# Kernel tuning notes

Hardware: AMD Instinct MI355X
Metric: run time of the kernel (lower is better)

The kernel has to match this reference:

```python
import jax, jax.numpy as jnp
import numpy as np

B, T, I, H, L, O = 256, 512, 5, 100, 5, 3
BN_EPS = 1e-5


def _lstm_layer(xs, W_ih, W_hh, bias):
    """xs: [B,T,in] -> hidden seq [B,T,H]. PyTorch gate order i,f,g,o."""
    Bv = xs.shape[0]
    Hd = W_hh.shape[1]
    h0 = jnp.zeros((Bv, Hd), xs.dtype)
    c0 = jnp.zeros((Bv, Hd), xs.dtype)

    def step(carry, x_t):
        h, c = carry
        gates = x_t @ W_ih.T + h @ W_hh.T + bias  # [B,4H]
        i, f, g, o = jnp.split(gates, 4, axis=-1)
        i = jax.nn.sigmoid(i)
        f = jax.nn.sigmoid(f)
        g = jnp.tanh(g)
        o = jax.nn.sigmoid(o)
        c = f * c + i * g
        h = o * jnp.tanh(c)
        return (h, c), h

    _, hs = jax.lax.scan(step, (h0, c0), xs.transpose(1, 0, 2))  # hs: [T,B,H]
    return hs.transpose(1, 0, 2)


def setup_inputs() -> dict:
    key = jax.random.key(0)
    ks = jax.random.split(key, 12)
    s = 0.1  # weight scale to keep gates in a reasonable range
    return {
        "x": jax.random.normal(ks[0], (B, T, I), jnp.float32),
        "W_ih0": jax.random.normal(ks[1], (4 * H, I), jnp.float32) * s,
        "W_hh0": jax.random.normal(ks[2], (4 * H, H), jnp.float32) * s,
        "b0": jax.random.normal(ks[3], (4 * H,), jnp.float32) * s,
        "W_ih": jax.random.normal(ks[4], (L - 1, 4 * H, H), jnp.float32) * s,
        "W_hh": jax.random.normal(ks[5], (L - 1, 4 * H, H), jnp.float32) * s,
        "b": jax.random.normal(ks[6], (L - 1, 4 * H), jnp.float32) * s,
        "gamma": jnp.ones((H,), jnp.float32),
        "beta": jnp.zeros((H,), jnp.float32),
        "run_mean": jnp.zeros((H,), jnp.float32),
        "run_var": jnp.ones((H,), jnp.float32),
        "W1": jax.random.normal(ks[7], (H, H), jnp.float32) * s,
        "b1": jnp.zeros((H,), jnp.float32),
        "W2": jax.random.normal(ks[8], (H, H), jnp.float32) * s,
        "b2": jnp.zeros((H,), jnp.float32),
        "W3": jax.random.normal(ks[9], (O, H), jnp.float32) * s,
        "b3": jnp.zeros((O,), jnp.float32),
    }


def reference(x, W_ih0, W_hh0, b0, W_ih, W_hh, b,
              gamma, beta, run_mean, run_var,
              W1, b1, W2, b2, W3, b3):
    # 5-layer stacked LSTM (batch_first)
    h = _lstm_layer(x, W_ih0, W_hh0, b0)
    for l in range(L - 1):
        h = _lstm_layer(h, W_ih[l], W_hh[l], b[l])
    # dropout (eval mode -> identity), take last timestep
    last = h[:, -1, :]  # [B,H]
    # BatchNorm1d, eval mode (running statistics)
    xn = (last - run_mean) * jax.lax.rsqrt(run_var + BN_EPS) * gamma + beta
    # 3-layer MLP head with ReLU
    y = jax.nn.relu(xn @ W1.T + b1)
    y = jax.nn.relu(y @ W2.T + b2)
    return y @ W3.T + b3  # [B,O]
```

## Files before the change

### kernel.cpp

```cpp
#include <hip/hip_runtime.h>

#define NT 1024
#define TSEQ 512

typedef float float2v __attribute__((ext_vector_type(2)));

__device__ __forceinline__ float sigmoid_(float x) { return 1.0f / (1.0f + __expf(-x)); }
__device__ __forceinline__ float tanh_(float x) { return 1.0f - 2.0f / (1.0f + __expf(2.0f * x)); }

extern "C" __global__ void prep_weights(const float* __restrict__ Wih0,
                                        const float* __restrict__ Whh0,
                                        const float* __restrict__ WihL,
                                        const float* __restrict__ WhhL,
                                        float4* __restrict__ wbuf) {
    int gid = blockIdx.x * 256 + threadIdx.x;
    if (gid >= 102400) return;
    int tid = gid & 1023;
    int lgq = gid >> 10;
    int gq = lgq % 20;
    int l = lgq / 20;
    int g = gq / 5, q = gq % 5;
    float tmp[4] = {0.f, 0.f, 0.f, 0.f};
    if (tid < 1000) {
        int f = tid / 100, rg = tid % 100;
        int row = g * 100 + rg;
        int k0 = 20 * f + 4 * q;
        for (int c = 0; c < 4; ++c) {
            int k = k0 + c;
            float w = 0.f;
            if (l == 0) {
                if (k < 5) w = Wih0[row * 5 + k];
                else if (k < 105) w = Whh0[row * 100 + (k - 5)];
            } else {
                if (k < 100) w = WihL[(l - 1) * 40000 + row * 100 + k];
                else w = WhhL[(l - 1) * 40000 + row * 100 + (k - 100)];
            }
            tmp[c] = w;
        }
    }
    wbuf[gid] = make_float4(tmp[0], tmp[1], tmp[2], tmp[3]);
}

template <int IN, bool FIRST, bool STORE>
__device__ void run_layer(const float4* __restrict__ wl, const float* __restrict__ bL,
                          const float* __restrict__ xsrc, float* __restrict__ hdst,
                          int b, int tid, int f, int rg, bool real,
                          float* xh, float4* part4) {
    float2v w[40];
#pragma unroll
    for (int g = 0; g < 4; ++g) {
#pragma unroll
        for (int q = 0; q < 5; ++q) {
            float4 t = wl[(g * 5 + q) * 1024 + tid];
            w[g * 10 + 2 * q]     = (float2v){t.x, t.y};
            w[g * 10 + 2 * q + 1] = (float2v){t.z, t.w};
        }
    }
    float bi = 0.f, bf = 0.f, bg = 0.f, bo = 0.f;
    if (tid < 100) {
        bi = bL[tid]; bf = bL[100 + tid]; bg = bL[200 + tid]; bo = bL[300 + tid];
    }

    if (tid < 256) xh[tid] = 0.f;
    __syncthreads();
    if (FIRST) {
        if (tid < 5) xh[tid] = xsrc[b * TSEQ * 5 + tid];
    } else {
        if (tid < 25) ((float4*)xh)[tid] = ((const float4*)xsrc)[b * TSEQ * 25 + tid];
    }
    __syncthreads();

    const float4* xv4 = (const float4*)xh + f * 5;
    float c = 0.f, hprev = 0.f;

    for (int t = 0; t < TSEQ; ++t) {
        if (STORE) {
            if (tid < 100 && t > 0) hdst[(b * TSEQ + (t - 1)) * 100 + tid] = hprev;
        }
        int tn = (t + 1 < TSEQ) ? (t + 1) : (TSEQ - 1);
        float pfs = 0.f;
        float4 pf4 = {0.f, 0.f, 0.f, 0.f};
        if (FIRST) {
            if (tid >= 128 && tid < 133) pfs = xsrc[(b * TSEQ + tn) * 5 + (tid - 128)];
        } else {
            if (tid >= 128 && tid < 153) pf4 = ((const float4*)xsrc)[(b * TSEQ + tn) * 25 + (tid - 128)];
        }

        float2v a0 = {0.f, 0.f}, a1 = {0.f, 0.f}, a2 = {0.f, 0.f}, a3 = {0.f, 0.f};
#pragma unroll
        for (int q = 0; q < 5; ++q) {
            float4 xq = xv4[q];
            float2v xlo = (float2v){xq.x, xq.y};
            float2v xhi = (float2v){xq.z, xq.w};
            a0 = __builtin_elementwise_fma(w[2 * q],      xlo, a0);
            a0 = __builtin_elementwise_fma(w[2 * q + 1],  xhi, a0);
            a1 = __builtin_elementwise_fma(w[10 + 2 * q],     xlo, a1);
            a1 = __builtin_elementwise_fma(w[10 + 2 * q + 1], xhi, a1);
            a2 = __builtin_elementwise_fma(w[20 + 2 * q],     xlo, a2);
            a2 = __builtin_elementwise_fma(w[20 + 2 * q + 1], xhi, a2);
            a3 = __builtin_elementwise_fma(w[30 + 2 * q],     xlo, a3);
            a3 = __builtin_elementwise_fma(w[30 + 2 * q + 1], xhi, a3);
        }
        if (real) {
            part4[f * 100 + rg] = make_float4(a0.x + a0.y, a1.x + a1.y,
                                              a2.x + a2.y, a3.x + a3.y);
        }
        __syncthreads();

        if (tid < 100) {
            float4 s = part4[tid];
#pragma unroll
            for (int ff = 1; ff < 10; ++ff) {
                float4 tt = part4[ff * 100 + tid];
                s.x += tt.x; s.y += tt.y; s.z += tt.z; s.w += tt.w;
            }
            float gi = sigmoid_(s.x + bi);
            float gf = sigmoid_(s.y + bf);
            float gg = tanh_(s.z + bg);
            float go = sigmoid_(s.w + bo);
            c = gf * c + gi * gg;
            float hv = go * tanh_(c);
            xh[IN + tid] = hv;
            hprev = hv;
        }
        if (FIRST) {
            if (tid >= 128 && tid < 133) xh[tid - 128] = pfs;
        } else {
            if (tid >= 128 && tid < 153) ((float4*)xh)[tid - 128] = pf4;
        }
        __syncthreads();
    }
    if (STORE) {
        if (tid < 100) hdst[(b * TSEQ + TSEQ - 1) * 100 + tid] = hprev;
    }
}

extern "C" __global__ void __launch_bounds__(NT, 4)
gesture_lstm_kernel(const float* __restrict__ x,
                    const float4* __restrict__ wbuf,
                    const float* __restrict__ b0, const float* __restrict__ bLv,
                    const float* __restrict__ gamma, const float* __restrict__ beta,
                    const float* __restrict__ rmean, const float* __restrict__ rvar,
                    const float* __restrict__ W1, const float* __restrict__ b1,
                    const float* __restrict__ W2, const float* __restrict__ b2,
                    const float* __restrict__ W3, const float* __restrict__ b3,
                    float* __restrict__ out, float* __restrict__ hseq) {
    __shared__ __align__(16) float xh[256];
    __shared__ __align__(16) float4 part4[1000];
    __shared__ __align__(16) float hw[10000];

    int tid = threadIdx.x;
    int b = blockIdx.x;
    int f = tid / 100;
    int rg = tid % 100;
    bool real = tid < 1000;

    run_layer<5,   true,  true >(wbuf + 0 * 20480, b0,         x,    hseq, b, tid, f, rg, real, xh, part4);
    run_layer<100, false, true >(wbuf + 1 * 20480, bLv + 0,    hseq, hseq, b, tid, f, rg, real, xh, part4);
    run_layer<100, false, true >(wbuf + 2 * 20480, bLv + 400,  hseq, hseq, b, tid, f, rg, real, xh, part4);
    run_layer<100, false, true >(wbuf + 3 * 20480, bLv + 800,  hseq, hseq, b, tid, f, rg, real, xh, part4);
    run_layer<100, false, false>(wbuf + 4 * 20480, bLv + 1200, hseq, hseq, b, tid, f, rg, real, xh, part4);

    float* fcbuf = (float*)part4;
    if (tid < 100) {
        float hv = xh[100 + tid];
        xh[tid] = (hv - rmean[tid]) * rsqrtf(rvar[tid] + 1e-5f) * gamma[tid] + beta[tid];
    }
    __syncthreads();

    for (int i = tid; i < 2500; i += NT) ((float4*)hw)[i] = ((const float4*)W1)[i];
    __syncthreads();
    if (tid < 100) {
        float acc = b1[tid];
#pragma unroll
        for (int k = 0; k < 100; ++k) acc = fmaf(hw[tid * 100 + k], xh[k], acc);
        fcbuf[tid] = fmaxf(acc, 0.0f);
    }
    __syncthreads();

    for (int i = tid; i < 2500; i += NT) ((float4*)hw)[i] = ((const float4*)W2)[i];
    __syncthreads();
    if (tid < 100) {
        float acc = b2[tid];
#pragma unroll
        for (int k = 0; k < 100; ++k) acc = fmaf(hw[tid * 100 + k], fcbuf[k], acc);
        fcbuf[400 + tid] = fmaxf(acc, 0.0f);
    }
    __syncthreads();

    if (tid < 3) {
        float acc = b3[tid];
#pragma unroll
        for (int k = 0; k < 100; ++k) acc = fmaf(W3[tid * 100 + k], fcbuf[400 + k], acc);
        out[b * 3 + tid] = acc;
    }
}

extern "C" void kernel_launch(void* const* d_in, const int* in_sizes, int n_in,
                              void* d_out, int out_size, void* d_ws, size_t ws_size,
                              hipStream_t stream) {
    const float* x     = (const float*)d_in[0];
    const float* Wih0  = (const float*)d_in[1];
    const float* Whh0  = (const float*)d_in[2];
    const float* b0    = (const float*)d_in[3];
    const float* WihL  = (const float*)d_in[4];
    const float* WhhL  = (const float*)d_in[5];
    const float* bLv   = (const float*)d_in[6];
    const float* gamma = (const float*)d_in[7];
    const float* beta  = (const float*)d_in[8];
    const float* rmean = (const float*)d_in[9];
    const float* rvar  = (const float*)d_in[10];
    const float* W1    = (const float*)d_in[11];
    const float* b1    = (const float*)d_in[12];
    const float* W2    = (const float*)d_in[13];
    const float* b2    = (const float*)d_in[14];
    const float* W3    = (const float*)d_in[15];
    const float* b3    = (const float*)d_in[16];

    float4* wbuf = (float4*)d_ws;
    float* hseq  = (float*)((char*)d_ws + 102400 * 16);

    prep_weights<<<dim3(400), dim3(256), 0, stream>>>(Wih0, Whh0, WihL, WhhL, wbuf);
    gesture_lstm_kernel<<<dim3(256), dim3(NT), 0, stream>>>(
        x, wbuf, b0, bLv, gamma, beta, rmean, rvar, W1, b1, W2, b2, W3, b3,
        (float*)d_out, hseq);
}
```

Baseline: 2.433 ms.

## Halve LSTM workgroup to 512 threads with 40-wide K slices

Reworks the per-sample LSTM workgroup from 1024 to 512 threads. Each thread now holds 80 float2 weight registers covering a 40-wide K slice, so the cross-slice reduction sums 5 partials instead of 10. The input-projection slices read x_t directly from global memory into registers, prefetched one step ahead, instead of staging it through shared memory. A lighter custom barrier replaces __syncthreads, and hidden-state stores are issued per step by the owner threads. The aim is to cut reduction and barrier cost per timestep, at the price of heavier register pressure (launch bounds lowered to 2) and more serial FMA work per thread.

```diff
diff --git a/kernel.cpp b/kernel.cpp
--- a/kernel.cpp
+++ b/kernel.cpp
@@ -1,12 +1,18 @@
 #include <hip/hip_runtime.h>
 
-#define NT 1024
+#define NT 512
 #define TSEQ 512
 
 typedef float float2v __attribute__((ext_vector_type(2)));
 
 __device__ __forceinline__ float sigmoid_(float x) { return 1.0f / (1.0f + __expf(-x)); }
 __device__ __forceinline__ float tanh_(float x) { return 1.0f - 2.0f / (1.0f + __expf(2.0f * x)); }
+
+__device__ __forceinline__ void wg_barrier() {
+    asm volatile("s_waitcnt lgkmcnt(0)" ::: "memory");
+    __builtin_amdgcn_s_barrier();
+    asm volatile("" ::: "memory");
+}
 
 extern "C" __global__ void prep_weights(const float* __restrict__ Wih0,
                                         const float* __restrict__ Whh0,
@@ -15,22 +21,22 @@
                                         float4* __restrict__ wbuf) {
     int gid = blockIdx.x * 256 + threadIdx.x;
     if (gid >= 102400) return;
-    int tid = gid & 1023;
-    int lgq = gid >> 10;
-    int gq = lgq % 20;
-    int l = lgq / 20;
-    int g = gq / 5, q = gq % 5;
+    int tid = gid & 511;
+    int lgq = gid >> 9;
+    int gq = lgq % 40;
+    int l = lgq / 40;
+    int g = gq / 10, q = gq % 10;
     float tmp[4] = {0.f, 0.f, 0.f, 0.f};
-    if (tid < 1000) {
+    if (tid < 500) {
         int f = tid / 100, rg = tid % 100;
         int row = g * 100 + rg;
-        int k0 = 20 * f + 4 * q;
+        int k0 = 40 * f + 4 * q;
         for (int c = 0; c < 4; ++c) {
             int k = k0 + c;
             float w = 0.f;
             if (l == 0) {
                 if (k < 5) w = Wih0[row * 5 + k];
-                else if (k < 105) w = Whh0[row * 100 + (k - 5)];
+                else if (k >= 20 && k < 120) w = Whh0[row * 100 + (k - 20)];
             } else {
                 if (k < 100) w = WihL[(l - 1) * 40000 + row * 100 + k];
                 else w = WhhL[(l - 1) * 40000 + row * 100 + (k - 100)];
@@ -41,101 +47,147 @@
     wbuf[gid] = make_float4(tmp[0], tmp[1], tmp[2], tmp[3]);
 }
 
-template <int IN, bool FIRST, bool STORE>
-__device__ void run_layer(const float4* __restrict__ wl, const float* __restrict__ bL,
-                          const float* __restrict__ xsrc, float* __restrict__ hdst,
-                          int b, int tid, int f, int rg, bool real,
-                          float* xh, float4* part4) {
-    float2v w[40];
-#pragma unroll
-    for (int g = 0; g < 4; ++g) {
-#pragma unroll
-        for (int q = 0; q < 5; ++q) {
-            float4 t = wl[(g * 5 + q) * 1024 + tid];
-            w[g * 10 + 2 * q]     = (float2v){t.x, t.y};
-            w[g * 10 + 2 * q + 1] = (float2v){t.z, t.w};
-        }
-    }
+#define STEP_Q(Q, XQ) { float4 xq_ = (XQ); \
+    float2v xlo = (float2v){xq_.x, xq_.y}; \
+    float2v xhi = (float2v){xq_.z, xq_.w}; \
+    a0 = __builtin_elementwise_fma(w[2*(Q)],      xlo, a0); \
+    a0 = __builtin_elementwise_fma(w[2*(Q)+1],    xhi, a0); \
+    a1 = __builtin_elementwise_fma(w[20+2*(Q)],   xlo, a1); \
+    a1 = __builtin_elementwise_fma(w[20+2*(Q)+1], xhi, a1); \
+    a2 = __builtin_elementwise_fma(w[40+2*(Q)],   xlo, a2); \
+    a2 = __builtin_elementwise_fma(w[40+2*(Q)+1], xhi, a2); \
+    a3 = __builtin_elementwise_fma(w[60+2*(Q)],   xlo, a3); \
+    a3 = __builtin_elementwise_fma(w[60+2*(Q)+1], xhi, a3); }
+
+template <bool FIRST, bool STORE>
+__device__ __forceinline__ void run_layer(const float4* __restrict__ wl,
+                                          const float* __restrict__ bL,
+                                          const float* __restrict__ xg,
+                                          float* __restrict__ hdst,
+                                          int b, int tid,
+                                          float* __restrict__ xh,
+                                          float4* __restrict__ part4) {
+    for (int i = tid; i < 192; i += NT) xh[i] = 0.f;
+
+    float2v w[80];
+#pragma unroll
+    for (int g = 0; g < 4; ++g)
+#pragma unroll
+        for (int q = 0; q < 10; ++q) {
+            float4 t4 = wl[(g * 10 + q) * 512 + tid];
+            w[g * 20 + 2 * q]     = (float2v){t4.x, t4.y};
+            w[g * 20 + 2 * q + 1] = (float2v){t4.z, t4.w};
+        }
+
+    int f = tid / 100; if (f > 4) f = 4;
+    int rg = tid % 100;
+    bool real = tid < 500;
+    bool owner = (tid >= 400 && tid < 500);
+    int cu = tid - 400;
     float bi = 0.f, bf = 0.f, bg = 0.f, bo = 0.f;
-    if (tid < 100) {
-        bi = bL[tid]; bf = bL[100 + tid]; bg = bL[200 + tid]; bo = bL[300 + tid];
-    }
-
-    if (tid < 256) xh[tid] = 0.f;
-    __syncthreads();
+    if (owner) { bi = bL[cu]; bf = bL[100 + cu]; bg = bL[200 + cu]; bo = bL[300 + cu]; }
+
+    const float4* xh4 = (const float4*)xh;
+    int nG;
+    const float4* xv4;
+    const float* grow;
     if (FIRST) {
-        if (tid < 5) xh[tid] = xsrc[b * TSEQ * 5 + tid];
+        nG  = (f == 0) ? 5 : 0;
+        xv4 = xh4 + (f == 0 ? 0 : 10 * f - 5);
+        grow = xg + (size_t)b * TSEQ * 5;
     } else {
-        if (tid < 25) ((float4*)xh)[tid] = ((const float4*)xsrc)[b * TSEQ * 25 + tid];
-    }
-    __syncthreads();
-
-    const float4* xv4 = (const float4*)xh + f * 5;
-    float c = 0.f, hprev = 0.f;
+        nG  = (f <= 1) ? 10 : (f == 2 ? 5 : 0);
+        xv4 = xh4 + (f == 2 ? 0 : 10 * f - 25);
+        grow = xg + (size_t)b * TSEQ * 100;
+    }
+
+    __syncthreads();
+
+    float4 gx[10];
+    float px[5];
+    auto issue = [&](int t) {
+        if (FIRST) {
+            if (nG == 5) {
+                const float* r = grow + t * 5;
+                px[0] = r[0]; px[1] = r[1]; px[2] = r[2]; px[3] = r[3]; px[4] = r[4];
+            }
+        } else {
+            if (nG == 10) {
+                const float4* r = (const float4*)(grow + t * 100) + f * 10;
+#pragma unroll
+                for (int q = 0; q < 10; ++q) gx[q] = r[q];
+            } else if (nG == 5) {
+                const float4* r = (const float4*)(grow + t * 100) + 20;
+#pragma unroll
+                for (int q = 0; q < 5; ++q) gx[q] = r[q];
+            }
+        }
+    };
+    issue(0);
+
+    float c = 0.f;
 
     for (int t = 0; t < TSEQ; ++t) {
-        if (STORE) {
-            if (tid < 100 && t > 0) hdst[(b * TSEQ + (t - 1)) * 100 + tid] = hprev;
-        }
-        int tn = (t + 1 < TSEQ) ? (t + 1) : (TSEQ - 1);
-        float pfs = 0.f;
-        float4 pf4 = {0.f, 0.f, 0.f, 0.f};
+        float2v a0 = {0.f, 0.f}, a1 = {0.f, 0.f}, a2 = {0.f, 0.f}, a3 = {0.f, 0.f};
+
         if (FIRST) {
-            if (tid >= 128 && tid < 133) pfs = xsrc[(b * TSEQ + tn) * 5 + (tid - 128)];
+            if (nG == 5) {
+                STEP_Q(0, make_float4(px[0], px[1], px[2], px[3]));
+                STEP_Q(1, make_float4(px[4], 0.f, 0.f, 0.f));
+#pragma unroll
+                for (int q = 5; q < 10; ++q) STEP_Q(q, xv4[q - 5]);
+            } else {
+#pragma unroll
+                for (int q = 0; q < 10; ++q) STEP_Q(q, xv4[q]);
+            }
         } else {
-            if (tid >= 128 && tid < 153) pf4 = ((const float4*)xsrc)[(b * TSEQ + tn) * 25 + (tid - 128)];
-        }
-
-        float2v a0 = {0.f, 0.f}, a1 = {0.f, 0.f}, a2 = {0.f, 0.f}, a3 = {0.f, 0.f};
-#pragma unroll
-        for (int q = 0; q < 5; ++q) {
-            float4 xq = xv4[q];
-            float2v xlo = (float2v){xq.x, xq.y};
-            float2v xhi = (float2v){xq.z, xq.w};
-            a0 = __builtin_elementwise_fma(w[2 * q],      xlo, a0);
-            a0 = __builtin_elementwise_fma(w[2 * q + 1],  xhi, a0);
-            a1 = __builtin_elementwise_fma(w[10 + 2 * q],     xlo, a1);
-            a1 = __builtin_elementwise_fma(w[10 + 2 * q + 1], xhi, a1);
-            a2 = __builtin_elementwise_fma(w[20 + 2 * q],     xlo, a2);
-            a2 = __builtin_elementwise_fma(w[20 + 2 * q + 1], xhi, a2);
-            a3 = __builtin_elementwise_fma(w[30 + 2 * q],     xlo, a3);
-            a3 = __builtin_elementwise_fma(w[30 + 2 * q + 1], xhi, a3);
-        }
-        if (real) {
-            part4[f * 100 + rg] = make_float4(a0.x + a0.y, a1.x + a1.y,
-                                              a2.x + a2.y, a3.x + a3.y);
-        }
-        __syncthreads();
-
-        if (tid < 100) {
-            float4 s = part4[tid];
-#pragma unroll
-            for (int ff = 1; ff < 10; ++ff) {
-                float4 tt = part4[ff * 100 + tid];
-                s.x += tt.x; s.y += tt.y; s.z += tt.z; s.w += tt.w;
-            }
-            float gi = sigmoid_(s.x + bi);
-            float gf = sigmoid_(s.y + bf);
-            float gg = tanh_(s.z + bg);
-            float go = sigmoid_(s.w + bo);
+            if (nG == 10) {
+#pragma unroll
+                for (int q = 0; q < 10; ++q) STEP_Q(q, gx[q]);
+            } else if (nG == 5) {
+#pragma unroll
+                for (int q = 0; q < 5; ++q) STEP_Q(q, gx[q]);
+#pragma unroll
+                for (int q = 5; q < 10; ++q) STEP_Q(q, xv4[q - 5]);
+            } else {
+#pragma unroll
+                for (int q = 0; q < 10; ++q) STEP_Q(q, xv4[q]);
+            }
+        }
+
+        int tn = (t + 1 < TSEQ) ? (t + 1) : t;
+        issue(tn);
+
+        if (real) part4[f * 100 + rg] = make_float4(a0.x + a0.y, a1.x + a1.y,
+                                                    a2.x + a2.y, a3.x + a3.y);
+        wg_barrier();
+
+        if (owner) {
+            float4 p = part4[cu];
+            float2v sA = (float2v){p.x, p.y};
+            float2v sB = (float2v){p.z, p.w};
+#pragma unroll
+            for (int ff = 1; ff < 5; ++ff) {
+                float4 p2 = part4[ff * 100 + cu];
+                sA += (float2v){p2.x, p2.y};
+                sB += (float2v){p2.z, p2.w};
+            }
+            float gi = sigmoid_(sA.x + bi);
+            float gf = sigmoid_(sA.y + bf);
+            float gg = tanh_(sB.x + bg);
+            float go = sigmoid_(sB.y + bo);
             c = gf * c + gi * gg;
             float hv = go * tanh_(c);
-            xh[IN + tid] = hv;
-            hprev = hv;
-        }
-        if (FIRST) {
-            if (tid >= 128 && tid < 133) xh[tid - 128] = pfs;
-        } else {
-            if (tid >= 128 && tid < 153) ((float4*)xh)[tid - 128] = pf4;
-        }
-        __syncthreads();
-    }
-    if (STORE) {
-        if (tid < 100) hdst[(b * TSEQ + TSEQ - 1) * 100 + tid] = hprev;
-    }
-}
-
-extern "C" __global__ void __launch_bounds__(NT, 4)
+            xh[cu] = hv;
+            if (STORE) hdst[((size_t)b * TSEQ + t) * 100 + cu] = hv;
+        }
+        wg_barrier();
+    }
+}
+
+#undef STEP_Q
+
+extern "C" __global__ void __launch_bounds__(NT, 2)
 gesture_lstm_kernel(const float* __restrict__ x,
                     const float4* __restrict__ wbuf,
                     const float* __restrict__ b0, const float* __restrict__ bLv,
@@ -145,25 +197,22 @@
                     const float* __restrict__ W2, const float* __restrict__ b2,
                     const float* __restrict__ W3, const float* __restrict__ b3,
                     float* __restrict__ out, float* __restrict__ hseq) {
-    __shared__ __align__(16) float xh[256];
-    __shared__ __align__(16) float4 part4[1000];
+    __shared__ __align__(16) float xh[192];
+    __shared__ __align__(16) float4 part4[500];
     __shared__ __align__(16) float hw[10000];
 
     int tid = threadIdx.x;
     int b = blockIdx.x;
-    int f = tid / 100;
-    int rg = tid % 100;
-    bool real = tid < 1000;
-
-    run_layer<5,   true,  true >(wbuf + 0 * 20480, b0,         x,    hseq, b, tid, f, rg, real, xh, part4);
-    run_layer<100, false, true >(wbuf + 1 * 20480, bLv + 0,    hseq, hseq, b, tid, f, rg, real, xh, part4);
-    run_layer<100, false, true >(wbuf + 2 * 20480, bLv + 400,  hseq, hseq, b, tid, f, rg, real, xh, part4);
-    run_layer<100, false, true >(wbuf + 3 * 20480, bLv + 800,  hseq, hseq, b, tid, f, rg, real, xh, part4);
-    run_layer<100, false, false>(wbuf + 4 * 20480, bLv + 1200, hseq, hseq, b, tid, f, rg, real, xh, part4);
+
+    run_layer<true,  true >(wbuf + 0 * 20480, b0,         x,    hseq, b, tid, xh, part4);
+    run_layer<false, true >(wbuf + 1 * 20480, bLv + 0,    hseq, hseq, b, tid, xh, part4);
+    run_layer<false, true >(wbuf + 2 * 20480, bLv + 400,  hseq, hseq, b, tid, xh, part4);
+    run_layer<false, true >(wbuf + 3 * 20480, bLv + 800,  hseq, hseq, b, tid, xh, part4);
+    run_layer<false, false>(wbuf + 4 * 20480, bLv + 1200, hseq, hseq, b, tid, xh, part4);
 
     float* fcbuf = (float*)part4;
     if (tid < 100) {
-        float hv = xh[100 + tid];
+        float hv = xh[tid];
         xh[tid] = (hv - rmean[tid]) * rsqrtf(rvar[tid] + 1e-5f) * gamma[tid] + beta[tid];
     }
     __syncthreads();
```

Result: slower. 3.049 ms (+25.3%).

## Read previous-layer hidden sequence directly from global and relax step barriers

Applied to the files above, without the earlier changes.

For layers after the first, the threads that handle the input half of the gate dot product now load the previous layer's hidden state for step t straight from global memory. This replaces the old scheme that prefetched it into LDS one step ahead, so the LDS region now holds only the recurrent h at offset 0. Hidden states are written to the output sequence at every step instead of one step late. The per-step __syncthreads is replaced by an LDS-only waitcnt plus s_barrier, so the barrier no longer waits on outstanding global loads and stores. The trade-off is that global-load latency may now land on the per-step critical path for the input-half threads.

```diff
diff --git a/kernel.cpp b/kernel.cpp
--- a/kernel.cpp
+++ b/kernel.cpp
@@ -7,6 +7,11 @@
 
 __device__ __forceinline__ float sigmoid_(float x) { return 1.0f / (1.0f + __expf(-x)); }
 __device__ __forceinline__ float tanh_(float x) { return 1.0f - 2.0f / (1.0f + __expf(2.0f * x)); }
+
+__device__ __forceinline__ void wg_barrier() {
+    asm volatile("s_waitcnt lgkmcnt(0)" ::: "memory");
+    __builtin_amdgcn_s_barrier();
+}
 
 extern "C" __global__ void prep_weights(const float* __restrict__ Wih0,
                                         const float* __restrict__ Whh0,
@@ -41,6 +46,18 @@
     wbuf[gid] = make_float4(tmp[0], tmp[1], tmp[2], tmp[3]);
 }
 
+#define STEP_Q(Q, XQ) { float4 xq_ = (XQ); \
+    float2v xlo = (float2v){xq_.x, xq_.y}; \
+    float2v xhi = (float2v){xq_.z, xq_.w}; \
+    a0 = __builtin_elementwise_fma(w[2*(Q)],      xlo, a0); \
+    a0 = __builtin_elementwise_fma(w[2*(Q)+1],    xhi, a0); \
+    a1 = __builtin_elementwise_fma(w[10+2*(Q)],   xlo, a1); \
+    a1 = __builtin_elementwise_fma(w[10+2*(Q)+1], xhi, a1); \
+    a2 = __builtin_elementwise_fma(w[20+2*(Q)],   xlo, a2); \
+    a2 = __builtin_elementwise_fma(w[20+2*(Q)+1], xhi, a2); \
+    a3 = __builtin_elementwise_fma(w[30+2*(Q)],   xlo, a3); \
+    a3 = __builtin_elementwise_fma(w[30+2*(Q)+1], xhi, a3); }
+
 template <int IN, bool FIRST, bool STORE>
 __device__ void run_layer(const float4* __restrict__ wl, const float* __restrict__ bL,
                           const float* __restrict__ xsrc, float* __restrict__ hdst,
@@ -65,47 +82,40 @@
     __syncthreads();
     if (FIRST) {
         if (tid < 5) xh[tid] = xsrc[b * TSEQ * 5 + tid];
-    } else {
-        if (tid < 25) ((float4*)xh)[tid] = ((const float4*)xsrc)[b * TSEQ * 25 + tid];
-    }
-    __syncthreads();
-
-    const float4* xv4 = (const float4*)xh + f * 5;
-    float c = 0.f, hprev = 0.f;
+    }
+    __syncthreads();
+
+    int fh = FIRST ? f : (f >= 5 ? f - 5 : 0);
+    const float4* xv4 = (const float4*)xh + fh * 5;
+    const float* grow = FIRST ? nullptr : (xsrc + (size_t)b * TSEQ * 100);
+
+    float c = 0.f;
 
     for (int t = 0; t < TSEQ; ++t) {
-        if (STORE) {
-            if (tid < 100 && t > 0) hdst[(b * TSEQ + (t - 1)) * 100 + tid] = hprev;
-        }
-        int tn = (t + 1 < TSEQ) ? (t + 1) : (TSEQ - 1);
+        float2v a0 = {0.f, 0.f}, a1 = {0.f, 0.f}, a2 = {0.f, 0.f}, a3 = {0.f, 0.f};
+
         float pfs = 0.f;
-        float4 pf4 = {0.f, 0.f, 0.f, 0.f};
         if (FIRST) {
+            int tn = (t + 1 < TSEQ) ? (t + 1) : (TSEQ - 1);
             if (tid >= 128 && tid < 133) pfs = xsrc[(b * TSEQ + tn) * 5 + (tid - 128)];
+#pragma unroll
+            for (int q = 0; q < 5; ++q) STEP_Q(q, xv4[q]);
         } else {
-            if (tid >= 128 && tid < 153) pf4 = ((const float4*)xsrc)[(b * TSEQ + tn) * 25 + (tid - 128)];
-        }
-
-        float2v a0 = {0.f, 0.f}, a1 = {0.f, 0.f}, a2 = {0.f, 0.f}, a3 = {0.f, 0.f};
-#pragma unroll
-        for (int q = 0; q < 5; ++q) {
-            float4 xq = xv4[q];
-            float2v xlo = (float2v){xq.x, xq.y};
-            float2v xhi = (float2v){xq.z, xq.w};
-            a0 = __builtin_elementwise_fma(w[2 * q],      xlo, a0);
-            a0 = __builtin_elementwise_fma(w[2 * q + 1],  xhi, a0);
-            a1 = __builtin_elementwise_fma(w[10 + 2 * q],     xlo, a1);
-            a1 = __builtin_elementwise_fma(w[10 + 2 * q + 1], xhi, a1);
-            a2 = __builtin_elementwise_fma(w[20 + 2 * q],     xlo, a2);
-            a2 = __builtin_elementwise_fma(w[20 + 2 * q + 1], xhi, a2);
-            a3 = __builtin_elementwise_fma(w[30 + 2 * q],     xlo, a3);
-            a3 = __builtin_elementwise_fma(w[30 + 2 * q + 1], xhi, a3);
-        }
+            if (f < 5) {
+                const float4* r = (const float4*)(grow + (size_t)t * 100) + f * 5;
+                float4 g0 = r[0], g1 = r[1], g2 = r[2], g3 = r[3], g4 = r[4];
+                STEP_Q(0, g0); STEP_Q(1, g1); STEP_Q(2, g2); STEP_Q(3, g3); STEP_Q(4, g4);
+            } else {
+#pragma unroll
+                for (int q = 0; q < 5; ++q) STEP_Q(q, xv4[q]);
+            }
+        }
+
         if (real) {
             part4[f * 100 + rg] = make_float4(a0.x + a0.y, a1.x + a1.y,
                                               a2.x + a2.y, a3.x + a3.y);
         }
-        __syncthreads();
+        wg_barrier();
 
         if (tid < 100) {
             float4 s = part4[tid];
@@ -121,19 +131,16 @@
             c = gf * c + gi * gg;
             float hv = go * tanh_(c);
             xh[IN + tid] = hv;
-            hprev = hv;
+            if (STORE) hdst[((size_t)b * TSEQ + t) * 100 + tid] = hv;
         }
         if (FIRST) {
             if (tid >= 128 && tid < 133) xh[tid - 128] = pfs;
-        } else {
-            if (tid >= 128 && tid < 153) ((float4*)xh)[tid - 128] = pf4;
-        }
-        __syncthreads();
-    }
-    if (STORE) {
-        if (tid < 100) hdst[(b * TSEQ + TSEQ - 1) * 100 + tid] = hprev;
-    }
-}
+        }
+        wg_barrier();
+    }
+}
+
+#undef STEP_Q
 
 extern "C" __global__ void __launch_bounds__(NT, 4)
 gesture_lstm_kernel(const float* __restrict__ x,
@@ -155,15 +162,15 @@
     int rg = tid % 100;
     bool real = tid < 1000;
 
-    run_layer<5,   true,  true >(wbuf + 0 * 20480, b0,         x,    hseq, b, tid, f, rg, real, xh, part4);
-    run_layer<100, false, true >(wbuf + 1 * 20480, bLv + 0,    hseq, hseq, b, tid, f, rg, real, xh, part4);
-    run_layer<100, false, true >(wbuf + 2 * 20480, bLv + 400,  hseq, hseq, b, tid, f, rg, real, xh, part4);
-    run_layer<100, false, true >(wbuf + 3 * 20480, bLv + 800,  hseq, hseq, b, tid, f, rg, real, xh, part4);
-    run_layer<100, false, false>(wbuf + 4 * 20480, bLv + 1200, hseq, hseq, b, tid, f, rg, real, xh, part4);
+    run_layer<5, true,  true >(wbuf + 0 * 20480, b0,         x,    hseq, b, tid, f, rg, real, xh, part4);
+    run_layer<0, false, true >(wbuf + 1 * 20480, bLv + 0,    hseq, hseq, b, tid, f, rg, real, xh, part4);
+    run_layer<0, false, true >(wbuf + 2 * 20480, bLv + 400,  hseq, hseq, b, tid, f, rg, real, xh, part4);
+    run_layer<0, false, true >(wbuf + 3 * 20480, bLv + 800,  hseq, hseq, b, tid, f, rg, real, xh, part4);
+    run_layer<0, false, false>(wbuf + 4 * 20480, bLv + 1200, hseq, hseq, b, tid, f, rg, real, xh, part4);
 
     float* fcbuf = (float*)part4;
     if (tid < 100) {
-        float hv = xh[100 + tid];
+        float hv = xh[tid];
         xh[tid] = (hv - rmean[tid]) * rsqrtf(rvar[tid] + 1e-5f) * gamma[tid] + beta[tid];
     }
     __syncthreads();
```

Result: slower. 2.651 ms (+9.0%).
